# Kernel optimization log

Measured on AMD Instinct MI355X. Metric: run time of the kernel, lower is better.

Reference implementation:

```python
import jax, jax.numpy as jnp
import numpy as np

RES = (8, 16, 16, 16)   # (t, d, h, w) control-point resolution
NDIM = 32               # channels per control point
B = 65536               # number of query coordinates


def _pad_axis(g, ax):
    # Linear extrapolation padding (one control point each side), as in
    # torch_cubic_spline_grids.pad_grids: edge gradient is continued outward.
    first = 2.0 * jnp.take(g, 0, axis=ax) - jnp.take(g, 1, axis=ax)
    last = 2.0 * jnp.take(g, -1, axis=ax) - jnp.take(g, -2, axis=ax)
    return jnp.concatenate(
        [jnp.expand_dims(first, ax), g, jnp.expand_dims(last, ax)], axis=ax
    )


def _bspline_weights(t):
    # Uniform cubic B-spline basis: [1,t,t^2,t^3] @ (1/6)[[1,4,1,0],[-3,0,3,0],[3,-6,3,0],[-1,3,-3,1]]
    t2 = t * t
    t3 = t2 * t
    w0 = (1.0 - 3.0 * t + 3.0 * t2 - t3) / 6.0
    w1 = (4.0 - 6.0 * t2 + 3.0 * t3) / 6.0
    w2 = (1.0 + 3.0 * t + 3.0 * t2 - 3.0 * t3) / 6.0
    w3 = t3 / 6.0
    return jnp.stack([w0, w1, w2, w3], axis=-1)  # (b, 4)


def setup_inputs() -> dict:
    key = jax.random.key(0)
    k1, k2 = jax.random.split(key)
    u = jax.random.uniform(k1, (B, 4), dtype=jnp.float32)  # coords in [0,1)
    grid = jax.random.normal(k2, (*RES, NDIM), dtype=jnp.float32)  # learned param
    return {"u": u, "grid": grid}


def reference(u, grid):
    # grid: (T, D, H, W, C); u: (b, 4) in [0,1] over (t, d, h, w)
    T, D, H, W, C = grid.shape
    gp = grid
    for ax in range(4):
        gp = _pad_axis(gp, ax)  # (T+2, D+2, H+2, W+2, C)
    Dp, Hp, Wp = D + 2, H + 2, W + 2

    sizes = jnp.asarray([T, D, H, W], dtype=u.dtype)
    s = u * (sizes - 1.0)                       # continuous control-point index
    i = jnp.clip(jnp.floor(s), 0.0, sizes - 2.0)  # lower knot, clamped so u=1 works
    t = s - i                                   # fractional position in [0,1]
    i = i.astype(jnp.int32)

    offs = jnp.arange(4, dtype=jnp.int32)
    # padded-grid indices of the 4 control points per dim: original i-1..i+2 -> i..i+3
    it = i[:, 0, None] + offs   # (b, 4)
    idd = i[:, 1, None] + offs
    ih = i[:, 2, None] + offs
    iw = i[:, 3, None] + offs

    # flat indices into padded grid, (b, 4, 4, 4, 4)
    flat = ((it[:, :, None, None, None] * Dp + idd[:, None, :, None, None]) * Hp
            + ih[:, None, None, :, None]) * Wp + iw[:, None, None, None, :]
    pts = gp.reshape(-1, C)[flat]  # (b, 4, 4, 4, 4, C) gathered control points

    wt = _bspline_weights(t[:, 0])
    wd = _bspline_weights(t[:, 1])
    wh = _bspline_weights(t[:, 2])
    ww = _bspline_weights(t[:, 3])

    # separable tensor-product weighting, reduced dim-by-dim by einsum
    return jnp.einsum('bijklc,bi,bj,bk,bl->bc', pts, wt, wd, wh, ww)
```

## Files before the change

kernel.cpp:

```cpp
#include <hip/hip_runtime.h>

#define NT 8
#define ND 16
#define NH 16
#define NW 16
#define NC 32
#define NB 65536
#define NCELLS (5 * 13 * 13)
#define CAP 512
#define CHUNKQ 32
#define MAXCHUNKS (NCELLS + NB / CHUNKQ)

typedef _Float16 f16x8 __attribute__((ext_vector_type(8)));
typedef _Float16 half2v __attribute__((ext_vector_type(2)));
typedef float f32x16 __attribute__((ext_vector_type(16)));
typedef __attribute__((ext_vector_type(8))) _Float16 half8;

template <int N>
__device__ __forceinline__ int span_base(float u) {
    float s = u * (float)(N - 1);
    float fi = fminf(fmaxf(floorf(s), 0.0f), (float)(N - 2));
    int i = (int)fi;
    return (i == 0) ? 0 : ((i == N - 2) ? (N - 4) : (i - 1));
}

template <int N>
__device__ __forceinline__ void dim_setup_span(float u, int& b, float w[4]) {
    float s = u * (float)(N - 1);
    float fi = fminf(fmaxf(floorf(s), 0.0f), (float)(N - 2));
    float t = s - fi;
    int i = (int)fi;
    float t2 = t * t, t3 = t2 * t;
    const float c6 = 1.0f / 6.0f;
    float w0 = (1.0f - 3.0f * t + 3.0f * t2 - t3) * c6;
    float w1 = (4.0f - 6.0f * t2 + 3.0f * t3) * c6;
    float w2 = (1.0f + 3.0f * t + 3.0f * t2 - 3.0f * t3) * c6;
    float w3 = t3 * c6;
    if (i == 0) {
        b = 0;
        w[0] = w1 + 2.0f * w0; w[1] = w2 - w0; w[2] = w3; w[3] = 0.0f;
    } else if (i == N - 2) {
        b = N - 4;
        w[0] = 0.0f; w[1] = w0; w[2] = w1 - w3; w[3] = w2 + 2.0f * w3;
    } else {
        b = i - 1;
        w[0] = w0; w[1] = w1; w[2] = w2; w[3] = w3;
    }
}

__global__ __launch_bounds__(512) void zero_meta_kernel(uint4* __restrict__ p) {
    p[threadIdx.x] = make_uint4(0, 0, 0, 0);
}

__global__ __launch_bounds__(256) void prep_kernel(
    const float* __restrict__ g, _Float16* __restrict__ gT,
    const float4* __restrict__ u4, int* __restrict__ count,
    int* __restrict__ perm, uint2* __restrict__ chunks,
    int* __restrict__ nchunks) {
    __shared__ int lhist[NCELLS];
    __shared__ int lbase[NCELLS];

    int b = blockIdx.x;
    int t = threadIdx.x;
    if (b < 256) {
        int idx = b * 256 + t;
        int row = idx >> 5;
        int c = idx & 31;
        const float* src = g + row * 512 + c;
        union { _Float16 h[16]; uint4 u[2]; } outv;
#pragma unroll
        for (int w = 0; w < 16; ++w) outv.h[w] = (_Float16)src[w * 32];
        uint4* dst = (uint4*)(gT + (size_t)row * 512 + c * 16);
        dst[0] = outv.u[0];
        dst[1] = outv.u[1];
    } else {
        for (int c = t; c < NCELLS; c += 256) lhist[c] = 0;
        __syncthreads();

        int q = (b - 256) * 256 + t;
        float4 uu = u4[q];
        int bt = span_base<NT>(uu.x);
        int bd = span_base<ND>(uu.y);
        int bh = span_base<NH>(uu.z);
        int cell = (bt * 13 + bd) * 13 + bh;
        int lrank = atomicAdd(&lhist[cell], 1);
        __syncthreads();

        for (int c = t; c < NCELLS; c += 256) {
            int n = lhist[c];
            lbase[c] = n ? atomicAdd(&count[c], n) : 0;
        }
        __syncthreads();

        int slot = lbase[cell] + lrank;
        if (slot < CAP) {
            perm[cell * CAP + slot] = q;
            if ((slot & (CHUNKQ - 1)) == 0) {
                int cid = atomicAdd(nchunks, 1);
                uint2 rec;
                rec.x = (unsigned)(cell * CAP + slot);
                rec.y = (unsigned)cell | ((unsigned)(slot / CHUNKQ) << 16);
                chunks[cid] = rec;
            }
        }
    }
}

__global__ __launch_bounds__(64) void spline4d_mfma_kernel(
    const float* __restrict__ u, const f16x8* __restrict__ gT,
    const int* __restrict__ count, const int* __restrict__ perm,
    const uint2* __restrict__ chunks, const int* __restrict__ nchunks,
    float* __restrict__ out) {
    if ((int)blockIdx.x >= *nchunks) return;

    uint2 rec = chunks[blockIdx.x];
    int start = (int)rec.x;
    int cell = (int)(rec.y & 0xffffu);
    int k32 = (int)(rec.y >> 16);
    int n = min(count[cell], CAP);
    int len = min(CHUNKQ, n - k32 * CHUNKQ);

    int bt = cell / 169;
    int r0 = cell - bt * 169;
    int bd = r0 / 13;
    int bh = r0 - bd * 13;

    int lane = (int)threadIdx.x;
    int slot = lane & 31;
    int hi = lane >> 5;
    int c = lane & 31;

    int q = perm[start + ((slot < len) ? slot : 0)];
    float4 uu = reinterpret_cast<const float4*>(u)[q];

    int xbt, xbd, xbh, bw;
    float wtv[4], wdv[4], whv[4], wwv[4];
    dim_setup_span<NT>(uu.x, xbt, wtv);
    dim_setup_span<ND>(uu.y, xbd, wdv);
    dim_setup_span<NH>(uu.z, xbh, whv);
    dim_setup_span<NW>(uu.w, bw, wwv);
    if (slot >= len) {
        wwv[0] = wwv[1] = wwv[2] = wwv[3] = 0.0f;
    }

    half2v wf[4];
#pragma unroll
    for (int j2 = 0; j2 < 4; ++j2) {
        int w0 = hi * 8 + 2 * j2;
        int d0 = w0 - bw, d1 = w0 + 1 - bw;
        float v0 = (d0 == 0) ? wwv[0] : (d0 == 1) ? wwv[1]
                 : (d0 == 2) ? wwv[2] : (d0 == 3) ? wwv[3] : 0.0f;
        float v1 = (d1 == 0) ? wwv[0] : (d1 == 1) ? wwv[1]
                 : (d1 == 2) ? wwv[2] : (d1 == 3) ? wwv[3] : 0.0f;
        wf[j2][0] = (_Float16)v0;
        wf[j2][1] = (_Float16)v1;
    }

    const f16x8* gp = gT + (c * 2 + hi);
    int rbase0 = (bt * ND + bd) * NH + bh;

    f32x16 acc0, acc1, acc2, acc3;
#pragma unroll
    for (int e = 0; e < 16; ++e) { acc0[e] = 0.0f; acc1[e] = 0.0f;
                                   acc2[e] = 0.0f; acc3[e] = 0.0f; }

#pragma unroll
    for (int j = 0; j < 4; ++j) {
        float wd0 = wtv[0] * wdv[j];
        float wd1 = wtv[1] * wdv[j];
        float wd2 = wtv[2] * wdv[j];
        float wd3 = wtv[3] * wdv[j];
        int rj = rbase0 + j * NH;
#pragma unroll
        for (int k = 0; k < 4; ++k) {
            int r = rj + k;
            f16x8 B0 = gp[(r          ) * 64];
            f16x8 B1 = gp[(r +     256) * 64];
            f16x8 B2 = gp[(r + 2 * 256) * 64];
            f16x8 B3 = gp[(r + 3 * 256) * 64];
            float whk = whv[k];
            _Float16 h0 = (_Float16)(wd0 * whk);
            _Float16 h1 = (_Float16)(wd1 * whk);
            _Float16 h2 = (_Float16)(wd2 * whk);
            _Float16 h3 = (_Float16)(wd3 * whk);
            half2v b0 = {h0, h0}, b1 = {h1, h1}, b2 = {h2, h2}, b3 = {h3, h3};
            union { f16x8 v; half2v h[4]; } A0, A1, A2, A3;
#pragma unroll
            for (int m = 0; m < 4; ++m) {
                A0.h[m] = b0 * wf[m];
                A1.h[m] = b1 * wf[m];
                A2.h[m] = b2 * wf[m];
                A3.h[m] = b3 * wf[m];
            }
            acc0 = __builtin_amdgcn_mfma_f32_32x32x16_f16(A0.v, B0, acc0, 0, 0, 0);
            acc1 = __builtin_amdgcn_mfma_f32_32x32x16_f16(A1.v, B1, acc1, 0, 0, 0);
            acc2 = __builtin_amdgcn_mfma_f32_32x32x16_f16(A2.v, B2, acc2, 0, 0, 0);
            acc3 = __builtin_amdgcn_mfma_f32_32x32x16_f16(A3.v, B3, acc3, 0, 0, 0);
        }
    }

#pragma unroll
    for (int e = 0; e < 16; ++e)
        acc0[e] = (acc0[e] + acc1[e]) + (acc2[e] + acc3[e]);

#pragma unroll
    for (int reg = 0; reg < 16; ++reg) {
        int sreg = (reg & 3) + 8 * (reg >> 2) + 4 * hi;
        int qs = __shfl(q, sreg);
        if (sreg < len) out[(size_t)qs * NC + c] = acc0[reg];
    }
}

typedef __attribute__((ext_vector_type(4))) _Float16 half4;

union H8 {
    half8 v;
    half2v h2[4];
};

__global__ __launch_bounds__(256) void convert_fp16_kernel(
    const float4* __restrict__ g, half4* __restrict__ hg) {
    int i = blockIdx.x * blockDim.x + threadIdx.x;
    float4 v = g[i];
    half4 h;
    h[0] = (_Float16)v.x;
    h[1] = (_Float16)v.y;
    h[2] = (_Float16)v.z;
    h[3] = (_Float16)v.w;
    hg[i] = h;
}

__global__ __launch_bounds__(256) void spline4d_fp16_kernel(
    const float* __restrict__ u, const half8* __restrict__ grid,
    float4* __restrict__ out) {
    int tid = blockIdx.x * blockDim.x + threadIdx.x;
    int q = tid >> 4;
    int s = tid & 15;

    float4 uu = reinterpret_cast<const float4*>(u)[q];

    int bt, bd, bh, bw;
    float wtv[4], wdv[4], whv[4], wwv[4];
    dim_setup_span<NT>(uu.x, bt, wtv);
    dim_setup_span<ND>(uu.y, bd, wdv);
    dim_setup_span<NH>(uu.z, bh, whv);
    dim_setup_span<NW>(uu.w, bw, wwv);

    int wp = s >> 2;
    float wlane = (wp & 2) ? ((wp & 1) ? wwv[3] : wwv[2])
                           : ((wp & 1) ? wwv[1] : wwv[0]);

    half2v whW2[4];
#pragma unroll
    for (int k = 0; k < 4; ++k) {
        _Float16 h = (_Float16)(whv[k] * wlane);
        whW2[k][0] = h;
        whW2[k][1] = h;
    }

    int base = ((((bt * ND + bd) * NH + bh) * NW + bw) << 2) + s;

    float facc[8];
#pragma unroll
    for (int c = 0; c < 8; ++c) facc[c] = 0.0f;
    half2v a01 = {0, 0}, a23 = {0, 0}, a45 = {0, 0}, a67 = {0, 0};

#pragma unroll
    for (int i = 0; i < 4; ++i) {
#pragma unroll
        for (int j = 0; j < 4; ++j) {
            _Float16 wtdh = (_Float16)(wtv[i] * wdv[j]);
            half2v wtd2 = {wtdh, wtdh};
#pragma unroll
            for (int k = 0; k < 4; ++k) {
                int a = base + i * (4 * ND * NH * NW) + j * (4 * NH * NW) +
                        k * (4 * NW);
                H8 P;
                P.v = grid[a];
                half2v uw = wtd2 * whW2[k];
                a01 += P.h2[0] * uw;
                a23 += P.h2[1] * uw;
                a45 += P.h2[2] * uw;
                a67 += P.h2[3] * uw;
            }
        }
        if (i == 1 || i == 3) {
            facc[0] += (float)a01[0]; facc[1] += (float)a01[1];
            facc[2] += (float)a23[0]; facc[3] += (float)a23[1];
            facc[4] += (float)a45[0]; facc[5] += (float)a45[1];
            facc[6] += (float)a67[0]; facc[7] += (float)a67[1];
            a01 = (half2v){0, 0}; a23 = (half2v){0, 0};
            a45 = (half2v){0, 0}; a67 = (half2v){0, 0};
        }
    }

#pragma unroll
    for (int c = 0; c < 8; ++c) {
        facc[c] += __shfl_xor(facc[c], 4);
        facc[c] += __shfl_xor(facc[c], 8);
    }

    if (s < 4) {
        out[q * 8 + s * 2] = make_float4(facc[0], facc[1], facc[2], facc[3]);
        out[q * 8 + s * 2 + 1] = make_float4(facc[4], facc[5], facc[6], facc[7]);
    }
}

extern "C" void kernel_launch(void* const* d_in, const int* in_sizes, int n_in,
                              void* d_out, int out_size, void* d_ws, size_t ws_size,
                              hipStream_t stream) {
    const float* u = (const float*)d_in[0];
    const float* grid_f32 = (const float*)d_in[1];

    const size_t n_grid_floats = (size_t)NT * ND * NH * NW * NC;
    const size_t GT_BYTES = n_grid_floats * 2;

    char* ws = (char*)d_ws;
    const size_t OFF_COUNT = GT_BYTES;
    const size_t OFF_NCH = OFF_COUNT + 4096;
    const size_t OFF_CHUNKS = OFF_NCH + 4096;
    const size_t OFF_PERM = OFF_CHUNKS + 24576;
    const size_t NEED = OFF_PERM + (size_t)NCELLS * CAP * 4;

    if (ws_size >= NEED) {
        _Float16* gT = (_Float16*)ws;
        int* count = (int*)(ws + OFF_COUNT);
        int* nchunks = (int*)(ws + OFF_NCH);
        uint2* chunks = (uint2*)(ws + OFF_CHUNKS);
        int* perm = (int*)(ws + OFF_PERM);

        zero_meta_kernel<<<1, 512, 0, stream>>>((uint4*)(ws + OFF_COUNT));
        prep_kernel<<<512, 256, 0, stream>>>(
            grid_f32, gT, (const float4*)u, count, perm, chunks, nchunks);
        spline4d_mfma_kernel<<<MAXCHUNKS, 64, 0, stream>>>(
            u, (const f16x8*)gT, count, perm, chunks, nchunks, (float*)d_out);
    } else if (ws_size >= GT_BYTES) {
        half4* hgrid = (half4*)ws;
        int cvt_blocks = (int)(n_grid_floats / 4 / 256);
        convert_fp16_kernel<<<cvt_blocks, 256, 0, stream>>>(
            (const float4*)grid_f32, hgrid);
        int nblocks = NB * 16 / 256;
        spline4d_fp16_kernel<<<nblocks, 256, 0, stream>>>(
            u, (const half8*)hgrid, (float4*)d_out);
    }
}
```

Measured before the change: 38.33 us.

## Split each chunk's t-dimension work across two wavefronts with atomic accumulation

```diff
diff --git a/kernel.cpp b/kernel.cpp
--- a/kernel.cpp
+++ b/kernel.cpp
@@ -48,8 +48,14 @@
     }
 }
 
-__global__ __launch_bounds__(512) void zero_meta_kernel(uint4* __restrict__ p) {
-    p[threadIdx.x] = make_uint4(0, 0, 0, 0);
+__global__ __launch_bounds__(512) void zero_meta_out_kernel(
+    uint4* __restrict__ meta, uint4* __restrict__ outv) {
+    int b = blockIdx.x;
+    if (b == 0) {
+        meta[threadIdx.x] = make_uint4(0, 0, 0, 0);
+    } else {
+        outv[(size_t)(b - 1) * 512 + threadIdx.x] = make_uint4(0, 0, 0, 0);
+    }
 }
 
 __global__ __launch_bounds__(256) void prep_kernel(
@@ -111,9 +117,12 @@
     const int* __restrict__ count, const int* __restrict__ perm,
     const uint2* __restrict__ chunks, const int* __restrict__ nchunks,
     float* __restrict__ out) {
-    if ((int)blockIdx.x >= *nchunks) return;
-
-    uint2 rec = chunks[blockIdx.x];
+    int bx = (int)blockIdx.x;
+    if (bx >= 2 * *nchunks) return;
+    int chunk = bx >> 1;
+    int half = bx & 1;
+
+    uint2 rec = chunks[chunk];
     int start = (int)rec.x;
     int cell = (int)(rec.y & 0xffffu);
     int k32 = (int)(rec.y >> 16);
@@ -142,6 +151,9 @@
     if (slot >= len) {
         wwv[0] = wwv[1] = wwv[2] = wwv[3] = 0.0f;
     }
+
+    float wtA = half ? wtv[2] : wtv[0];
+    float wtB = half ? wtv[3] : wtv[1];
 
     half2v wf[4];
 #pragma unroll
@@ -157,57 +169,45 @@
     }
 
     const f16x8* gp = gT + (c * 2 + hi);
-    int rbase0 = (bt * ND + bd) * NH + bh;
-
-    f32x16 acc0, acc1, acc2, acc3;
-#pragma unroll
-    for (int e = 0; e < 16; ++e) { acc0[e] = 0.0f; acc1[e] = 0.0f;
-                                   acc2[e] = 0.0f; acc3[e] = 0.0f; }
+    int rbase = ((bt + 2 * half) * ND + bd) * NH + bh;
+
+    f32x16 accA, accB;
+#pragma unroll
+    for (int e = 0; e < 16; ++e) { accA[e] = 0.0f; accB[e] = 0.0f; }
 
 #pragma unroll
     for (int j = 0; j < 4; ++j) {
-        float wd0 = wtv[0] * wdv[j];
-        float wd1 = wtv[1] * wdv[j];
-        float wd2 = wtv[2] * wdv[j];
-        float wd3 = wtv[3] * wdv[j];
-        int rj = rbase0 + j * NH;
+        float wdA = wtA * wdv[j];
+        float wdB = wtB * wdv[j];
+        int rj = rbase + j * NH;
 #pragma unroll
         for (int k = 0; k < 4; ++k) {
             int r = rj + k;
-            f16x8 B0 = gp[(r          ) * 64];
-            f16x8 B1 = gp[(r +     256) * 64];
-            f16x8 B2 = gp[(r + 2 * 256) * 64];
-            f16x8 B3 = gp[(r + 3 * 256) * 64];
+            f16x8 B0 = gp[r * 64];
+            f16x8 B1 = gp[(r + 256) * 64];
             float whk = whv[k];
-            _Float16 h0 = (_Float16)(wd0 * whk);
-            _Float16 h1 = (_Float16)(wd1 * whk);
-            _Float16 h2 = (_Float16)(wd2 * whk);
-            _Float16 h3 = (_Float16)(wd3 * whk);
-            half2v b0 = {h0, h0}, b1 = {h1, h1}, b2 = {h2, h2}, b3 = {h3, h3};
-            union { f16x8 v; half2v h[4]; } A0, A1, A2, A3;
+            _Float16 hA = (_Float16)(wdA * whk);
+            _Float16 hB = (_Float16)(wdB * whk);
+            half2v bA = {hA, hA}, bB = {hB, hB};
+            union { f16x8 v; half2v h[4]; } A0, A1;
 #pragma unroll
             for (int m = 0; m < 4; ++m) {
-                A0.h[m] = b0 * wf[m];
-                A1.h[m] = b1 * wf[m];
-                A2.h[m] = b2 * wf[m];
-                A3.h[m] = b3 * wf[m];
+                A0.h[m] = bA * wf[m];
+                A1.h[m] = bB * wf[m];
             }
-            acc0 = __builtin_amdgcn_mfma_f32_32x32x16_f16(A0.v, B0, acc0, 0, 0, 0);
-            acc1 = __builtin_amdgcn_mfma_f32_32x32x16_f16(A1.v, B1, acc1, 0, 0, 0);
-            acc2 = __builtin_amdgcn_mfma_f32_32x32x16_f16(A2.v, B2, acc2, 0, 0, 0);
-            acc3 = __builtin_amdgcn_mfma_f32_32x32x16_f16(A3.v, B3, acc3, 0, 0, 0);
-        }
-    }
-
-#pragma unroll
-    for (int e = 0; e < 16; ++e)
-        acc0[e] = (acc0[e] + acc1[e]) + (acc2[e] + acc3[e]);
+            accA = __builtin_amdgcn_mfma_f32_32x32x16_f16(A0.v, B0, accA, 0, 0, 0);
+            accB = __builtin_amdgcn_mfma_f32_32x32x16_f16(A1.v, B1, accB, 0, 0, 0);
+        }
+    }
+
+#pragma unroll
+    for (int e = 0; e < 16; ++e) accA[e] += accB[e];
 
 #pragma unroll
     for (int reg = 0; reg < 16; ++reg) {
         int sreg = (reg & 3) + 8 * (reg >> 2) + 4 * hi;
         int qs = __shfl(q, sreg);
-        if (sreg < len) out[(size_t)qs * NC + c] = acc0[reg];
+        if (sreg < len) atomicAdd(&out[(size_t)qs * NC + c], accA[reg]);
     }
 }
 
@@ -329,10 +329,11 @@
         uint2* chunks = (uint2*)(ws + OFF_CHUNKS);
         int* perm = (int*)(ws + OFF_PERM);
 
-        zero_meta_kernel<<<1, 512, 0, stream>>>((uint4*)(ws + OFF_COUNT));
+        zero_meta_out_kernel<<<1025, 512, 0, stream>>>(
+            (uint4*)(ws + OFF_COUNT), (uint4*)d_out);
         prep_kernel<<<512, 256, 0, stream>>>(
             grid_f32, gT, (const float4*)u, count, perm, chunks, nchunks);
-        spline4d_mfma_kernel<<<MAXCHUNKS, 64, 0, stream>>>(
+        spline4d_mfma_kernel<<<2 * MAXCHUNKS, 64, 0, stream>>>(
             u, (const f16x8*)gT, count, perm, chunks, nchunks, (float*)d_out);
     } else if (ws_size >= GT_BYTES) {
         half4* hgrid = (half4*)ws;
```

Result: slower. 45.66 us (+19.1%).
